# Performance work log

Measured on AMD Instinct MI355X. Metric: run time of the kernel, lower is better.

The kernel has to match this reference:

```python
import jax, jax.numpy as jnp
import numpy as np

EMBED_DIM = 1024
NUM_HEADS = 16
HEAD_DIM = EMBED_DIM // NUM_HEADS
SEQ_LEN = 2048
BATCH = 2


def setup_inputs() -> dict:
    key = jax.random.key(0)
    ks = jax.random.split(key, 9)
    s = 1.0 / np.sqrt(EMBED_DIM)
    inputs = jax.random.normal(ks[0], (BATCH, SEQ_LEN, EMBED_DIM), dtype=jnp.float32)
    Wq = jax.random.uniform(ks[1], (EMBED_DIM, EMBED_DIM), jnp.float32, -s, s)
    bq = jax.random.uniform(ks[2], (EMBED_DIM,), jnp.float32, -s, s)
    Wk = jax.random.uniform(ks[3], (EMBED_DIM, EMBED_DIM), jnp.float32, -s, s)
    bk = jax.random.uniform(ks[4], (EMBED_DIM,), jnp.float32, -s, s)
    Wv = jax.random.uniform(ks[5], (EMBED_DIM, EMBED_DIM), jnp.float32, -s, s)
    bv = jax.random.uniform(ks[6], (EMBED_DIM,), jnp.float32, -s, s)
    Wo = jax.random.uniform(ks[7], (EMBED_DIM, EMBED_DIM), jnp.float32, -s, s)
    bo = jax.random.uniform(ks[8], (EMBED_DIM,), jnp.float32, -s, s)
    return {"inputs": inputs, "Wq": Wq, "bq": bq, "Wk": Wk, "bk": bk,
            "Wv": Wv, "bv": bv, "Wo": Wo, "bo": bo}


def reference(inputs, Wq, bq, Wk, bk, Wv, bv, Wo, bo):
    B, S, D = inputs.shape
    H, Hd = NUM_HEADS, HEAD_DIM

    def heads(x):  # [B,S,D] -> [B,H,S,Hd]
        return x.reshape(B, S, H, Hd).transpose(0, 2, 1, 3)

    q = heads(inputs @ Wq + bq)
    k = heads(inputs @ Wk + bk)
    v = heads(inputs @ Wv + bv)

    # [B,H,S,S] causal scores (naive, matching original module)
    scores = jnp.einsum('bhqd,bhkd->bhqk', q, k) * (Hd ** -0.5)
    causal = jnp.tril(jnp.ones((S, S), dtype=bool))
    scores = jnp.where(causal, scores, jnp.float32(-jnp.inf))
    attn = jax.nn.softmax(scores, axis=-1)

    out = jnp.einsum('bhqk,bhkd->bhqd', attn, v)
    out = out.transpose(0, 2, 1, 3).reshape(B, S, D)
    return out @ Wo + bo
```

## Files before the change

### kernel.cpp

```cpp
#include <hip/hip_runtime.h>
#include <stdint.h>
#include <stddef.h>

#define SEQ   2048
#define DIM   1024
#define NH    16
#define HD    64
#define MTOT  4096
#define LPAD  72
#define EPAD  136
#define FPAD  132

typedef __attribute__((ext_vector_type(8))) short short8;
typedef __attribute__((ext_vector_type(4))) float floatx4;
typedef __attribute__((ext_vector_type(16))) float floatx16;
typedef __attribute__((ext_vector_type(4))) float float4v;
typedef __attribute__((ext_vector_type(4))) unsigned short ushort4v;
typedef __attribute__((ext_vector_type(4))) unsigned int uint4v;

__device__ __forceinline__ floatx4 mfma_bf16(short8 a, short8 b, floatx4 c) {
    return __builtin_amdgcn_mfma_f32_16x16x32_bf16(a, b, c, 0, 0, 0);
}
__device__ __forceinline__ floatx16 mfma32(short8 a, short8 b, floatx16 c) {
    return __builtin_amdgcn_mfma_f32_32x32x16_bf16(a, b, c, 0, 0, 0);
}

__device__ __forceinline__ float b2f(unsigned short s) {
    unsigned int u = ((unsigned int)s) << 16;
    return __builtin_bit_cast(float, u);
}
__device__ __forceinline__ unsigned short f2b(float f) {
    unsigned int u = __builtin_bit_cast(unsigned int, f);
    u += 0x7fffu + ((u >> 16) & 1u);
    return (unsigned short)(u >> 16);
}
__device__ __forceinline__ unsigned int cvtpk(float lo, float hi) {
    unsigned int w;
    asm("v_cvt_pk_bf16_f32 %0, %1, %2" : "=v"(w) : "v"(lo), "v"(hi));
    return w;
}
__device__ __forceinline__ void swap32(unsigned int& a, unsigned int& b) {
    asm("v_permlane32_swap_b32 %0, %1" : "+v"(a), "+v"(b));
}
__device__ __forceinline__ short8 mk8(unsigned int a, unsigned int b,
                                      unsigned int c, unsigned int d) {
    uint4v u; u.x = a; u.y = b; u.z = c; u.w = d;
    return __builtin_bit_cast(short8, u);
}

__global__ __launch_bounds__(256) void cvt_f32_bf16(const float* __restrict__ in,
                                                    unsigned short* __restrict__ out) {
    const int i = (blockIdx.x * 256 + threadIdx.x) * 4;
    const float4v v = *(const float4v*)&in[i];
    ushort4v o;
    o.x = f2b(v.x); o.y = f2b(v.y); o.z = f2b(v.z); o.w = f2b(v.w);
    *(ushort4v*)&out[i] = o;
}

__global__ __launch_bounds__(256) void transpose_all(const float* __restrict__ w0,
                                                     const float* __restrict__ w1,
                                                     const float* __restrict__ w2,
                                                     const float* __restrict__ w3,
                                                     unsigned short* __restrict__ outbase) {
    __shared__ float t[64][65];
    const int z = blockIdx.z;
    const float* in = (z == 0) ? w0 : (z == 1) ? w1 : (z == 2) ? w2 : w3;
    unsigned short* out = outbase + (size_t)z * DIM * DIM;
    const int c0 = blockIdx.x * 64, r0 = blockIdx.y * 64;
    const int x = threadIdx.x, y = threadIdx.y;
#pragma unroll
    for (int i = 0; i < 64; i += 4)
        t[y + i][x] = in[(size_t)(r0 + y + i) * DIM + c0 + x];
    __syncthreads();
#pragma unroll
    for (int i = 0; i < 64; i += 4)
        out[(size_t)(c0 + y + i) * DIM + r0 + x] = f2b(t[x][y + i]);
}

__global__ __launch_bounds__(256) void gemm_fused(const unsigned short* __restrict__ A,
                                                  const unsigned short* __restrict__ WTbase,
                                                  const float* __restrict__ b0,
                                                  const float* __restrict__ b1,
                                                  const float* __restrict__ b2,
                                                  void* __restrict__ outbase,
                                                  int qkv) {
    __shared__ __attribute__((aligned(16))) unsigned short smem[2 * 128 * LPAD];
    unsigned short* As = smem;
    unsigned short* Bs = smem + 128 * LPAD;

    const int z = blockIdx.z;
    const unsigned short* BT = WTbase + (size_t)z * (DIM * DIM);
    const float* bias        = (z == 0) ? b0 : (z == 1) ? b1 : b2;
    const int mode = qkv ? ((z == 0) ? 1 : (z == 1) ? 3 : 4) : 0;
    float* Cf          = (float*)outbase;
    unsigned short* Cb = (unsigned short*)outbase + (size_t)z * ((size_t)MTOT * DIM);

    const int tid = threadIdx.x;
    const int w = tid >> 6, lane = tid & 63;
    const int quad = lane >> 4, l16 = lane & 15;
    const int wm = w >> 1, wn = w & 1;
    const int m0 = blockIdx.x * 128, n0 = blockIdx.y * 128;
    const int bb = m0 >> 11;

    floatx4 acc[4][4];
#pragma unroll
    for (int mi = 0; mi < 4; ++mi)
#pragma unroll
        for (int ni = 0; ni < 4; ++ni) acc[mi][ni] = (floatx4)0.0f;

    const int srow = tid >> 3, scol = (tid & 7) * 8;

    short8 pa[4], pb[4];
#pragma unroll
    for (int ch = 0; ch < 4; ++ch) {
        pa[ch] = *(const short8*)&A[(size_t)(m0 + ch * 32 + srow) * DIM + scol];
        pb[ch] = *(const short8*)&BT[(size_t)(n0 + ch * 32 + srow) * DIM + scol];
    }

    for (int k0 = 0;; k0 += 64) {
#pragma unroll
        for (int ch = 0; ch < 4; ++ch) {
            *(short8*)&As[(ch * 32 + srow) * LPAD + scol] = pa[ch];
            *(short8*)&Bs[(ch * 32 + srow) * LPAD + scol] = pb[ch];
        }
        __syncthreads();
        const bool more = (k0 + 64 < DIM);
        if (more) {
#pragma unroll
            for (int ch = 0; ch < 4; ++ch) {
                pa[ch] = *(const short8*)&A[(size_t)(m0 + ch * 32 + srow) * DIM + k0 + 64 + scol];
                pb[ch] = *(const short8*)&BT[(size_t)(n0 + ch * 32 + srow) * DIM + k0 + 64 + scol];
            }
        }
#pragma unroll
        for (int kk = 0; kk < 2; ++kk) {
            short8 a[4], b[4];
#pragma unroll
            for (int mi = 0; mi < 4; ++mi)
                a[mi] = *(const short8*)&As[(wm * 64 + mi * 16 + l16) * LPAD + kk * 32 + quad * 8];
#pragma unroll
            for (int ni = 0; ni < 4; ++ni)
                b[ni] = *(const short8*)&Bs[(wn * 64 + ni * 16 + l16) * LPAD + kk * 32 + quad * 8];
#pragma unroll
            for (int mi = 0; mi < 4; ++mi)
#pragma unroll
                for (int ni = 0; ni < 4; ++ni)
                    acc[mi][ni] = mfma_bf16(a[mi], b[ni], acc[mi][ni]);
        }
        if (!more) break;
        __syncthreads();
    }

    float bvv[4];
#pragma unroll
    for (int ni = 0; ni < 4; ++ni) bvv[ni] = bias[n0 + wn * 64 + ni * 16 + l16];

    if (mode == 0) {
        float* T = (float*)smem;
        for (int p = 0; p < 4; ++p) {
            __syncthreads();
            if (wm == (p >> 1)) {
                const int mib = (p & 1) * 2;
#pragma unroll
                for (int mm = 0; mm < 2; ++mm)
#pragma unroll
                    for (int ni = 0; ni < 4; ++ni)
#pragma unroll
                        for (int r = 0; r < 4; ++r)
                            T[(mm * 16 + quad * 4 + r) * FPAD + wn * 64 + ni * 16 + l16] =
                                acc[mib + mm][ni][r] + bvv[ni];
            }
            __syncthreads();
#pragma unroll
            for (int it = 0; it < 4; ++it) {
                const int c = it * 256 + tid;
                const int row = c >> 5, nof = (c & 31) * 4;
                *(float4v*)&Cf[(size_t)(m0 + p * 32 + row) * DIM + n0 + nof] =
                    *(const float4v*)&T[row * FPAD + nof];
            }
        }
    } else if (mode == 1) {
        unsigned short* T = smem;
        __syncthreads();
#pragma unroll
        for (int mi = 0; mi < 4; ++mi)
#pragma unroll
            for (int ni = 0; ni < 4; ++ni)
#pragma unroll
                for (int r = 0; r < 4; ++r)
                    T[(wm * 64 + mi * 16 + quad * 4 + r) * EPAD + wn * 64 + ni * 16 + l16] =
                        f2b(acc[mi][ni][r] + bvv[ni]);
        __syncthreads();
#pragma unroll
        for (int it = 0; it < 8; ++it) {
            const int c = it * 256 + tid;
            const int seg = c >> 3, d8 = (c & 7) * 8;
            const int mm = seg >> 1, hseg = seg & 1;
            const int h = (n0 >> 6) + hseg;
            const int s = (m0 & (SEQ - 1)) + mm;
            *(short8*)&Cb[((size_t)(bb * NH + h) * SEQ + s) * HD + d8] =
                *(const short8*)&T[mm * EPAD + hseg * 64 + d8];
        }
    } else if (mode == 3) {
        unsigned short* T = smem;
        __syncthreads();
#pragma unroll
        for (int mi = 0; mi < 4; ++mi)
#pragma unroll
            for (int ni = 0; ni < 4; ++ni)
#pragma unroll
                for (int r = 0; r < 4; ++r)
                    T[(wm * 64 + mi * 16 + quad * 4 + r) * EPAD + wn * 64 + ni * 16 + l16] =
                        f2b(acc[mi][ni][r] + bvv[ni]);
        __syncthreads();
#pragma unroll
        for (int it = 0; it < 8; ++it) {
            const int f = it * 256 + tid;
            const int ln = f & 63, fragid = f >> 6;
            const int h2 = fragid >> 4;
            const int jb = (fragid >> 2) & 3;
            const int c  = fragid & 3;
            const short8 v = *(const short8*)&T[(jb * 32 + (ln & 31)) * EPAD +
                                                h2 * 64 + c * 16 + (ln >> 5) * 8];
            const int bh = bb * NH + (n0 >> 6) + h2;
            const int jg = ((m0 & (SEQ - 1)) >> 5) + jb;
            *(short8*)&Cb[(((size_t)bh * 64 + jg) * 4 + c) * 512 + ln * 8] = v;
        }
    } else {
        unsigned short* T = smem;
        __syncthreads();
#pragma unroll
        for (int mi = 0; mi < 4; ++mi)
#pragma unroll
            for (int ni = 0; ni < 4; ++ni) {
                ushort4v pk;
#pragma unroll
                for (int r = 0; r < 4; ++r) pk[r] = f2b(acc[mi][ni][r] + bvv[ni]);
                *(ushort4v*)&T[(wn * 64 + ni * 16 + l16) * EPAD + wm * 64 + mi * 16 + quad * 4] = pk;
            }
        __syncthreads();
#pragma unroll
        for (int it = 0; it < 8; ++it) {
            const int f = it * 256 + tid;
            const int ln = f & 63, fragid = f >> 6;
            const int h2 = fragid >> 4;
            const int jb = (fragid >> 2) & 3;
            const int dk = fragid & 3;
            const int d0 = dk >> 1, kk = dk & 1;
            const short8 v = *(const short8*)&T[(h2 * 64 + d0 * 32 + (ln & 31)) * EPAD +
                                                jb * 32 + kk * 16 + (ln >> 5) * 8];
            const int bh = bb * NH + (n0 >> 6) + h2;
            const int jg = ((m0 & (SEQ - 1)) >> 5) + jb;
            *(short8*)&Cb[(((size_t)bh * 64 + jg) * 4 + dk) * 512 + ln * 8] = v;
        }
    }
}

__global__ __launch_bounds__(64) void attn_fwd(const unsigned short* __restrict__ Q,
                                               const unsigned short* __restrict__ KP,
                                               const unsigned short* __restrict__ VP,
                                               unsigned short* __restrict__ O) {
    __shared__ __attribute__((aligned(16))) unsigned short Os[32 * LPAD];
    __shared__ float Linv[32];

    const int bh = blockIdx.x;
    const int qc = (gridDim.y - 1) - blockIdx.y;
    const int lane = threadIdx.x;
    const int ql  = lane & 31;
    const int hi  = lane >> 5;
    const int hi4 = hi * 4;
    const int hi8 = hi * 8;

    const unsigned short* Qh  = Q  + (size_t)bh * SEQ * HD;
    const unsigned short* KPh = KP + (size_t)bh * (64 * 2048);
    const unsigned short* VPh = VP + (size_t)bh * (64 * 2048);
    const int q0 = qc * 32;

    short8 qf[4];
#pragma unroll
    for (int c = 0; c < 4; ++c) {
        short8 t = *(const short8*)(Qh + (size_t)(q0 + ql) * HD + c * 16 + hi8);
        short8 o;
#pragma unroll
        for (int e = 0; e < 8; ++e)
            o[e] = (short)f2b(b2f((unsigned short)t[e]) * 0.125f);
        qf[c] = o;
    }

    floatx16 o_acc0 = (floatx16)0.0f, o_acc1 = (floatx16)0.0f;
    float l0 = 0.0f, l1 = 0.0f;

#define LOADKV(KF, VF, JJ) do {                                              \
        const unsigned short* kb_ = KPh + (size_t)(JJ) * 2048 + lane * 8;    \
        const unsigned short* vb_ = VPh + (size_t)(JJ) * 2048 + lane * 8;    \
        _Pragma("unroll")                                                    \
        for (int c_ = 0; c_ < 4; ++c_) {                                     \
            KF[c_] = *(const short8*)(kb_ + c_ * 512);                       \
            VF[c_] = *(const short8*)(vb_ + c_ * 512);                       \
        }                                                                    \
    } while (0)

#define ATT_BLOCK(KF, VF, MASKED) do {                                       \
        floatx16 st_ = (floatx16)0.0f;                                       \
        _Pragma("unroll")                                                    \
        for (int c_ = 0; c_ < 4; ++c_) st_ = mfma32(KF[c_], qf[c_], st_);    \
        float p_[16];                                                        \
        _Pragma("unroll")                                                    \
        for (int r_ = 0; r_ < 16; ++r_) {                                    \
            float e_ = __expf(st_[r_]);                                      \
            if (MASKED)                                                      \
                e_ = (((r_ & 3) + 8 * (r_ >> 2) + hi4) > ql) ? 0.0f : e_;    \
            p_[r_] = e_;                                                     \
        }                                                                    \
        l0 += (p_[0] + p_[1]) + (p_[2] + p_[3]);                             \
        l1 += (p_[4] + p_[5]) + (p_[6] + p_[7]);                             \
        l0 += (p_[8] + p_[9]) + (p_[10] + p_[11]);                           \
        l1 += (p_[12] + p_[13]) + (p_[14] + p_[15]);                         \
        unsigned int w0_ = cvtpk(p_[0], p_[1]),   w2_ = cvtpk(p_[4], p_[5]); \
        unsigned int w1_ = cvtpk(p_[2], p_[3]),   w3_ = cvtpk(p_[6], p_[7]); \
        unsigned int w4_ = cvtpk(p_[8], p_[9]),   w6_ = cvtpk(p_[12], p_[13]); \
        unsigned int w5_ = cvtpk(p_[10], p_[11]), w7_ = cvtpk(p_[14], p_[15]); \
        swap32(w0_, w2_); swap32(w1_, w3_);                                  \
        swap32(w4_, w6_); swap32(w5_, w7_);                                  \
        const short8 pa0_ = mk8(w0_, w1_, w2_, w3_);                         \
        const short8 pa1_ = mk8(w4_, w5_, w6_, w7_);                         \
        o_acc0 = mfma32(pa0_, VF[0], o_acc0);                                \
        o_acc0 = mfma32(pa1_, VF[1], o_acc0);                                \
        o_acc1 = mfma32(pa0_, VF[2], o_acc1);                                \
        o_acc1 = mfma32(pa1_, VF[3], o_acc1);                                \
    } while (0)

    short8 kfA[4], vfA[4], kfB[4], vfB[4];
    LOADKV(kfA, vfA, 0);
    int j = 0;
    while (j + 2 <= qc) {
        LOADKV(kfB, vfB, j + 1);
        ATT_BLOCK(kfA, vfA, 0);
        LOADKV(kfA, vfA, j + 2);
        ATT_BLOCK(kfB, vfB, 0);
        j += 2;
    }
    if (j < qc) {
        LOADKV(kfB, vfB, qc);
        ATT_BLOCK(kfA, vfA, 0);
        ATT_BLOCK(kfB, vfB, 1);
    } else {
        ATT_BLOCK(kfA, vfA, 1);
    }

    float l = l0 + l1;
    l += __shfl_xor(l, 32, 64);
    const float inv = 1.0f / l;
    if (lane < 32) Linv[lane] = inv;
    __syncthreads();
#pragma unroll
    for (int r = 0; r < 16; ++r) {
        const int row = (r & 3) + 8 * (r >> 2) + hi4;
        const float iv = Linv[row];
        Os[row * LPAD + ql]      = f2b(o_acc0[r] * iv);
        Os[row * LPAD + 32 + ql] = f2b(o_acc1[r] * iv);
    }
    __syncthreads();
    const int bb = bh >> 4, h = bh & 15;
#pragma unroll
    for (int it = 0; it < 4; ++it) {
        const int row = it * 8 + (lane >> 3), d8 = (lane & 7) * 8;
        *(short8*)&O[(size_t)(bb * SEQ + q0 + row) * DIM + h * HD + d8] =
            *(const short8*)&Os[row * LPAD + d8];
    }
#undef LOADKV
#undef ATT_BLOCK
}

extern "C" void kernel_launch(void* const* d_in, const int* in_sizes, int n_in,
                              void* d_out, int out_size, void* d_ws, size_t ws_size,
                              hipStream_t stream) {
    const float* X  = (const float*)d_in[0];
    const float* Wq = (const float*)d_in[1];
    const float* bq = (const float*)d_in[2];
    const float* Wk = (const float*)d_in[3];
    const float* bk = (const float*)d_in[4];
    const float* Wv = (const float*)d_in[5];
    const float* bv = (const float*)d_in[6];
    const float* Wo = (const float*)d_in[7];
    const float* bo = (const float*)d_in[8];

    unsigned short* ws = (unsigned short*)d_ws;
    const size_t WSZ = (size_t)DIM * DIM;
    const size_t TSZ = (size_t)MTOT * DIM;
    unsigned short* WqT = ws;
    unsigned short* WoT = ws + 3 * WSZ;
    unsigned short* Qb  = ws + 4 * WSZ;
    unsigned short* Kp  = Qb + TSZ;
    unsigned short* Vp  = Kp + TSZ;
    unsigned short* Ob  = Vp + TSZ;

    unsigned short* Xb = (unsigned short*)d_out;

    cvt_f32_bf16<<<dim3(TSZ / 1024), 256, 0, stream>>>(X, Xb);

    transpose_all<<<dim3(16, 16, 4), dim3(64, 4), 0, stream>>>(Wq, Wk, Wv, Wo, WqT);

    gemm_fused<<<dim3(MTOT / 128, DIM / 128, 3), 256, 0, stream>>>(
        Xb, WqT, bq, bk, bv, (void*)Qb, 1);

    attn_fwd<<<dim3(2 * NH, SEQ / 32), 64, 0, stream>>>(Qb, Kp, Vp, Ob);

    gemm_fused<<<dim3(MTOT / 128, DIM / 128, 1), 256, 0, stream>>>(
        Ob, WoT, bo, bo, bo, d_out, 0);
}
```

Before: 186.3 us.

## Load GEMM tiles directly to LDS with XOR-swizzled layout

The projection GEMM's staging through registers (global load, then LDS store) is replaced by direct global-to-LDS loads of 16 bytes per lane. The padded LDS layout gives way to an unpadded 64-wide row with an XOR swizzle on 8-element chunks to avoid bank conflicts. This drops the register prefetch buffers and VGPR traffic. The explicit software prefetch overlap is lost, since loads now issue right before the barrier in each iteration, and the loop stays single-buffered.

Measured after the change: 171.2 us. 1.09x faster.

```diff
diff --git a/kernel.cpp b/kernel.cpp
--- a/kernel.cpp
+++ b/kernel.cpp
@@ -46,6 +46,11 @@
                                       unsigned int c, unsigned int d) {
     uint4v u; u.x = a; u.y = b; u.z = c; u.w = d;
     return __builtin_bit_cast(short8, u);
+}
+__device__ __forceinline__ void g2l16(const unsigned short* g, unsigned short* l) {
+    __builtin_amdgcn_global_load_lds(
+        (const __attribute__((address_space(1))) void*)g,
+        (__attribute__((address_space(3))) void*)l, 16, 0, 0);
 }
 
 __global__ __launch_bounds__(256) void cvt_f32_bf16(const float* __restrict__ in,
@@ -86,7 +91,7 @@
                                                   int qkv) {
     __shared__ __attribute__((aligned(16))) unsigned short smem[2 * 128 * LPAD];
     unsigned short* As = smem;
-    unsigned short* Bs = smem + 128 * LPAD;
+    unsigned short* Bs = smem + 128 * 64;
 
     const int z = blockIdx.z;
     const unsigned short* BT = WTbase + (size_t)z * (DIM * DIM);
@@ -108,46 +113,38 @@
 #pragma unroll
         for (int ni = 0; ni < 4; ++ni) acc[mi][ni] = (floatx4)0.0f;
 
-    const int srow = tid >> 3, scol = (tid & 7) * 8;
-
-    short8 pa[4], pb[4];
-#pragma unroll
-    for (int ch = 0; ch < 4; ++ch) {
-        pa[ch] = *(const short8*)&A[(size_t)(m0 + ch * 32 + srow) * DIM + scol];
-        pb[ch] = *(const short8*)&BT[(size_t)(n0 + ch * 32 + srow) * DIM + scol];
-    }
-
-    for (int k0 = 0;; k0 += 64) {
-#pragma unroll
-        for (int ch = 0; ch < 4; ++ch) {
-            *(short8*)&As[(ch * 32 + srow) * LPAD + scol] = pa[ch];
-            *(short8*)&Bs[(ch * 32 + srow) * LPAD + scol] = pb[ch];
-        }
-        __syncthreads();
-        const bool more = (k0 + 64 < DIM);
-        if (more) {
-#pragma unroll
-            for (int ch = 0; ch < 4; ++ch) {
-                pa[ch] = *(const short8*)&A[(size_t)(m0 + ch * 32 + srow) * DIM + k0 + 64 + scol];
-                pb[ch] = *(const short8*)&BT[(size_t)(n0 + ch * 32 + srow) * DIM + k0 + 64 + scol];
-            }
-        }
+    const int srow8 = lane >> 3;
+    const int sgs8  = ((lane & 7) ^ srow8) * 8;
+    const unsigned short* gA = &A [(size_t)(m0 + w * 8 + srow8) * DIM + sgs8];
+    const unsigned short* gB = &BT[(size_t)(n0 + w * 8 + srow8) * DIM + sgs8];
+
+    const int sx = l16 & 7;
+
+    for (int k0 = 0; ; k0 += 64) {
+#pragma unroll
+        for (int i = 0; i < 4; ++i) {
+            g2l16(gA + (size_t)i * (32 * DIM) + k0, &As[(i * 4 + w) * 512]);
+            g2l16(gB + (size_t)i * (32 * DIM) + k0, &Bs[(i * 4 + w) * 512]);
+        }
+        __syncthreads();
 #pragma unroll
         for (int kk = 0; kk < 2; ++kk) {
             short8 a[4], b[4];
 #pragma unroll
             for (int mi = 0; mi < 4; ++mi)
-                a[mi] = *(const short8*)&As[(wm * 64 + mi * 16 + l16) * LPAD + kk * 32 + quad * 8];
+                a[mi] = *(const short8*)&As[(wm * 64 + mi * 16 + l16) * 64 +
+                                            (((kk * 4) + quad) ^ sx) * 8];
 #pragma unroll
             for (int ni = 0; ni < 4; ++ni)
-                b[ni] = *(const short8*)&Bs[(wn * 64 + ni * 16 + l16) * LPAD + kk * 32 + quad * 8];
+                b[ni] = *(const short8*)&Bs[(wn * 64 + ni * 16 + l16) * 64 +
+                                            (((kk * 4) + quad) ^ sx) * 8];
 #pragma unroll
             for (int mi = 0; mi < 4; ++mi)
 #pragma unroll
                 for (int ni = 0; ni < 4; ++ni)
                     acc[mi][ni] = mfma_bf16(a[mi], b[ni], acc[mi][ni]);
         }
-        if (!more) break;
+        if (k0 + 64 >= DIM) break;
         __syncthreads();
     }
 
```
